# Kernel optimization log

Measured on AMD Instinct MI355X. Metric: run time of the kernel, lower is better.

Reference implementation:

```python
import jax, jax.numpy as jnp
import numpy as np

B, T, C, H = 4, 2048, 1024, 16
D = C // H

def setup_inputs() -> dict:
    key = jax.random.key(0)
    ks = jax.random.split(key, 9)
    s = 0.02
    return {
        "x": jax.random.normal(ks[0], (B, T, C), dtype=jnp.float32),
        "Wq": jax.random.normal(ks[1], (C, C), dtype=jnp.float32) * s,
        "bq": jnp.zeros((C,), dtype=jnp.float32),
        "Wk": jax.random.normal(ks[2], (C, C), dtype=jnp.float32) * s,
        "bk": jnp.zeros((C,), dtype=jnp.float32),
        "Wv": jax.random.normal(ks[3], (C, C), dtype=jnp.float32) * s,
        "bv": jnp.zeros((C,), dtype=jnp.float32),
        "Wo": jax.random.normal(ks[4], (C, C), dtype=jnp.float32) * s,
        "bo": jnp.zeros((C,), dtype=jnp.float32),
    }

def reference(x, Wq, bq, Wk, bk, Wv, bv, Wo, bo):
    # torch nn.Linear: y = x @ W.T + b
    q = x @ Wq.T + bq  # (B,T,C)
    k = x @ Wk.T + bk
    v = x @ Wv.T + bv
    # (B,H,T,D)
    q = q.reshape(B, T, H, D).transpose(0, 2, 1, 3)
    k = k.reshape(B, T, H, D).transpose(0, 2, 1, 3)
    v = v.reshape(B, T, H, D).transpose(0, 2, 1, 3)
    scale = 1.0 / jnp.sqrt(jnp.asarray(D, dtype=q.dtype))
    att = jnp.einsum("bhqd,bhkd->bhqk", q, k) * scale  # (B,H,T,T)
    causal = jnp.tril(jnp.ones((T, T), dtype=bool))
    att = jnp.where(causal[None, None], att, jnp.asarray(-jnp.inf, dtype=att.dtype))
    att = jax.nn.softmax(att, axis=-1)
    y = jnp.einsum("bhqk,bhkd->bhqd", att, v)  # (B,H,T,D)
    y = y.transpose(0, 2, 1, 3).reshape(B, T, C)
    return y @ Wo.T + bo
```

## Files before the change

### kernel.cpp

```cpp
#include <hip/hip_runtime.h>
#include <hip/hip_bf16.h>
#include <stdint.h>

typedef unsigned short u16;
typedef __bf16 bf16x8 __attribute__((ext_vector_type(8)));
typedef float f32x4 __attribute__((ext_vector_type(4)));
typedef float f32x16 __attribute__((ext_vector_type(16)));

#define NB 4
#define NT 2048
#define NC 1024
#define NH 16
#define ND 64
#define NM 8192
#define KVB 64

__device__ __forceinline__ u16 f2bf(float f) {
  union { float f; uint32_t u; } v; v.f = f;
  return (u16)((v.u + 0x7FFFu + ((v.u >> 16) & 1u)) >> 16);
}

__device__ __forceinline__ uint32_t pk2(float a, float b) {
  union { __hip_bfloat162 h; uint32_t u; } c;
  c.h = __float22bfloat162_rn(float2{a, b});
  return c.u;
}

__device__ __forceinline__ float fexp2(float x) {
#if __has_builtin(__builtin_amdgcn_exp2f)
  return __builtin_amdgcn_exp2f(x);
#else
  return exp2f(x);
#endif
}

__device__ __forceinline__ void g2l16(const void* g, void* l) {
  __builtin_amdgcn_global_load_lds((__attribute__((address_space(1))) const void*)g,
                                   (__attribute__((address_space(3))) void*)l,
                                   16, 0, 0);
}

__global__ __launch_bounds__(256) void cvt4(const float* __restrict__ in,
                                            u16* __restrict__ out, int n4) {
  int i = blockIdx.x * 256 + threadIdx.x;
  if (i >= n4) return;
  float4 v = ((const float4*)in)[i];
  ushort4 o;
  o.x = f2bf(v.x); o.y = f2bf(v.y); o.z = f2bf(v.z); o.w = f2bf(v.w);
  ((ushort4*)out)[i] = o;
}

__global__ __launch_bounds__(256) void cvtW(const float* __restrict__ w0,
                                            const float* __restrict__ w1,
                                            const float* __restrict__ w2,
                                            const float* __restrict__ w3,
                                            u16* o0, u16* o1, u16* o2, u16* o3) {
  const int y = blockIdx.y;
  const float* in = (y == 0) ? w0 : (y == 1) ? w1 : (y == 2) ? w2 : w3;
  u16* out = (y == 0) ? o0 : (y == 1) ? o1 : (y == 2) ? o2 : o3;
  int i = blockIdx.x * 256 + threadIdx.x;
  float4 v = ((const float4*)in)[i];
  ushort4 o;
  o.x = f2bf(v.x); o.y = f2bf(v.y); o.z = f2bf(v.z); o.w = f2bf(v.w);
  ((ushort4*)out)[i] = o;
}

template <int EPI>
__global__ __launch_bounds__(512, 6) void gemmQ(
    const u16* __restrict__ A,
    const u16* __restrict__ W0, const u16* __restrict__ W1, const u16* __restrict__ W2,
    const float* __restrict__ b0, const float* __restrict__ b1, const float* __restrict__ b2,
    void* o0, void* o1, void* o2, int M, int N, int K) {
  const int z = blockIdx.z;
  const u16* Bw = (z == 0) ? W0 : ((z == 1) ? W1 : W2);
  const float* bias = (z == 0) ? b0 : ((z == 1) ? b1 : b2);
  void* outp = (z == 0) ? o0 : ((z == 1) ? o1 : o2);

  __shared__ __align__(16) char SB[3 * 16384];

  const int nbn = N >> 7;
  const int lb = (blockIdx.x & 7) * (gridDim.x >> 3) + (blockIdx.x >> 3);
  const int m0 = (lb / nbn) << 7;
  const int n0 = (lb % nbn) << 7;
  const int t = threadIdx.x;
  const int wid = t >> 6, lane = t & 63;
  const int wm = wid >> 2, wn = wid & 3;
  const int lo = lane & 15, hi = lane >> 4;

  const int rw = t >> 2;
  const int chs = (((t & 3) ^ (rw & 3) ^ ((rw >> 2) & 3)) << 3);
  const u16* Asrc0 = A + (size_t)(m0 + rw) * K + chs;
  const u16* Bsrc0 = Bw + (size_t)(n0 + rw) * K + chs;
  const int ldsoff = t * 16;

  f32x4 acc[4][2];
#pragma unroll
  for (int f = 0; f < 4; ++f)
#pragma unroll
    for (int g = 0; g < 2; ++g) acc[f][g] = f32x4{0.f, 0.f, 0.f, 0.f};

  const int NTILES = K >> 5;

  auto STAGE = [&](int buf, int kt) {
    g2l16(Asrc0 + kt * 32, SB + buf * 16384 + ldsoff);
    g2l16(Bsrc0 + kt * 32, SB + buf * 16384 + 8192 + ldsoff);
  };

  STAGE(0, 0);
  STAGE(1, 1);

  int cur = 0;
  for (int kt = 0; kt < NTILES; ++kt) {
    if (kt == NTILES - 1)
      asm volatile("s_waitcnt vmcnt(0)" ::: "memory");
    else
      asm volatile("s_waitcnt vmcnt(2)" ::: "memory");
    __builtin_amdgcn_sched_barrier(0);
    asm volatile("s_barrier" ::: "memory");
    __builtin_amdgcn_sched_barrier(0);

    if (kt + 2 < NTILES) {
      int nb = cur + 2;
      if (nb >= 3) nb -= 3;
      STAGE(nb, kt + 2);
    }

    const char* Ab = SB + cur * 16384;
    const char* Bb = SB + cur * 16384 + 8192;
    bf16x8 af[4], bfr[2];
#pragma unroll
    for (int f = 0; f < 4; ++f) {
      const int row = wm * 64 + f * 16 + lo;
      af[f] = *(const bf16x8*)(Ab + row * 64 + ((hi ^ (row & 3) ^ ((row >> 2) & 3)) << 4));
    }
#pragma unroll
    for (int g = 0; g < 2; ++g) {
      const int row = wn * 32 + g * 16 + lo;
      bfr[g] = *(const bf16x8*)(Bb + row * 64 + ((hi ^ (row & 3) ^ ((row >> 2) & 3)) << 4));
    }
    __builtin_amdgcn_s_setprio(1);
#pragma unroll
    for (int f = 0; f < 4; ++f)
#pragma unroll
      for (int g = 0; g < 2; ++g)
        acc[f][g] = __builtin_amdgcn_mfma_f32_16x16x32_bf16(af[f], bfr[g],
                                                            acc[f][g], 0, 0, 0);
    __builtin_amdgcn_s_setprio(0);
    cur = (cur + 1 == 3) ? 0 : cur + 1;
  }

  const float scl = (EPI == 0 && z == 0) ? 0.125f * 1.44269504089f : 1.0f;
#pragma unroll
  for (int f = 0; f < 4; ++f) {
#pragma unroll
    for (int g = 0; g < 2; ++g) {
#pragma unroll
      for (int r = 0; r < 4; ++r) {
        const int rg = m0 + wm * 64 + f * 16 + hi * 4 + r;
        const int cg = n0 + wn * 32 + g * 16 + lo;
        const float v = (acc[f][g][r] + bias[cg]) * scl;
        if (EPI == 0) {
          const int bb = rg >> 11, tt = rg & (NT - 1);
          const int hh = cg >> 6, dd = cg & (ND - 1);
          size_t idx;
          if (z == 2)
            idx = ((size_t)(bb * NH + hh) * ND + dd) * NT + tt;
          else
            idx = ((size_t)(bb * NH + hh) * NT + tt) * ND + dd;
          ((u16*)outp)[idx] = f2bf(v);
        } else {
          ((float*)outp)[(size_t)rg * N + cg] = v;
        }
      }
    }
  }
}

__global__ __launch_bounds__(512, 4) void flash5(const u16* __restrict__ Q,
                                                 const u16* __restrict__ Kg,
                                                 const u16* __restrict__ Vtg,
                                                 u16* __restrict__ Y) {
  __shared__ __align__(16) char LDS[65536];

  const int n = blockIdx.x;
  const int xcd = n & 7, slot = n >> 3;
  const int bh = (xcd << 3) | (slot >> 3);
  const int pt = slot & 7;
  const int qtB = 15 - pt;
  const int bb = bh >> 4, hh = bh & (NH - 1);
  const int tid = threadIdx.x;
  const int lane = tid & 63;
  const int grp = tid >> 8;
  const int ws4 = (tid >> 6) & 3;
  const int ql = lane & 31, h5 = lane >> 5;
  const int swz = (ql & 7) << 4;

  const u16* Qb = Q + (size_t)bh * NT * ND;
  const u16* Kb = Kg + (size_t)bh * NT * ND;
  const u16* Vb = Vtg + (size_t)bh * ND * NT;

  const int ntA = 2 * pt + 2;
  const int kvb1 = 15 - 2 * pt;
  const int q0wB = (qtB << 7) + (ws4 << 5);

  int q0w = grp ? q0wB : (pt << 7) + (ws4 << 5);
  int qg = q0w + ql;

  bf16x8 qf[4];
#pragma unroll
  for (int s = 0; s < 4; ++s)
    qf[s] = *(const bf16x8*)(Qb + (size_t)qg * ND + s * 16 + h5 * 8);

  f32x16 O0 = 0.f, O1 = 0.f;
  float lr = 0.f;

  const int tl = tid & 255;
  char* myL = LDS + (grp << 15);

  auto kvof = [&](int it) {
    return grp ? (kvb1 + it) : (it < ntA ? it : it - ntA);
  };

  auto STAGE = [&](int buf, int kv) {
#pragma unroll
    for (int p = 0; p < 2; ++p) {
      const int c = tl + (p << 8);
      const int row = c >> 3;
      const int so = ((c & 7) << 4) ^ ((row & 7) << 4);
      g2l16((const char*)(Kb + (size_t)((kv << 6) + row) * ND) + so,
            myL + (buf << 14) + c * 16);
      g2l16((const char*)(Vb + (size_t)row * NT + (kv << 6)) + so,
            myL + (buf << 14) + 8192 + c * 16);
    }
  };

  auto WRITEY = [&](const f32x16& A0, const f32x16& A1, float inv, int qgl) {
    u16* Yb = Y + ((size_t)bb * NT + qgl) * NC + hh * ND;
#pragma unroll
    for (int rq = 0; rq < 16; rq += 4) {
      const int dbase = 2 * rq + 4 * h5;
      uint2 w2;
      w2.x = pk2(A0[rq] * inv, A0[rq + 1] * inv);
      w2.y = pk2(A0[rq + 2] * inv, A0[rq + 3] * inv);
      *(uint2*)(Yb + dbase) = w2;
      w2.x = pk2(A1[rq] * inv, A1[rq + 1] * inv);
      w2.y = pk2(A1[rq + 2] * inv, A1[rq + 3] * inv);
      *(uint2*)(Yb + 32 + dbase) = w2;
    }
  };

  STAGE(0, kvof(0));
  __syncthreads();

  for (int it = 0; it < 17; ++it) {
    const int buf = it & 1;
    if (it < 16) STAGE(buf ^ 1, kvof(it + 1));

    if (!grp && it == ntA) {
      const float lt = lr + __shfl_xor(lr, 32, 64);
      WRITEY(O0, O1, 1.f / lt, qg);
      O0 = 0.f; O1 = 0.f; lr = 0.f;
      q0w = q0wB; qg = q0w + ql;
#pragma unroll
      for (int s = 0; s < 4; ++s)
        qf[s] = *(const bf16x8*)(Qb + (size_t)qg * ND + s * 16 + h5 * 8);
    }

    const int kv0 = kvof(it) << 6;
    const char* Kc = myL + (buf << 14);
    const char* Vc = Kc + 8192;

    f32x16 Sa0 = 0.f, Sa1 = 0.f;
    __builtin_amdgcn_s_setprio(1);
#pragma unroll
    for (int s = 0; s < 4; ++s) {
      bf16x8 kf0 = *(const bf16x8*)(Kc + ql * 128 + ((s * 32 + h5 * 16) ^ swz));
      bf16x8 kf1 = *(const bf16x8*)(Kc + (32 + ql) * 128 + ((s * 32 + h5 * 16) ^ swz));
      Sa0 = __builtin_amdgcn_mfma_f32_32x32x16_bf16(kf0, qf[s], Sa0, 0, 0, 0);
      Sa1 = __builtin_amdgcn_mfma_f32_32x32x16_bf16(kf1, qf[s], Sa1, 0, 0, 0);
    }
    __builtin_amdgcn_s_setprio(0);

    if (kv0 + 63 > q0w) {
#pragma unroll
      for (int r = 0; r < 16; ++r) {
        const int kvb = kv0 + (r & 3) + 8 * (r >> 2) + 4 * h5;
        if (kvb > qg) Sa0[r] = -3e38f;
        if (kvb + 32 > qg) Sa1[r] = -3e38f;
      }
    }

    float t0 = 0.f, t1 = 0.f, t2 = 0.f, t3 = 0.f;
#pragma unroll
    for (int r = 0; r < 16; r += 4) {
      const float a0 = fexp2(Sa0[r]),     a1 = fexp2(Sa0[r + 1]);
      const float a2 = fexp2(Sa0[r + 2]), a3 = fexp2(Sa0[r + 3]);
      const float b0 = fexp2(Sa1[r]),     b1 = fexp2(Sa1[r + 1]);
      const float b2 = fexp2(Sa1[r + 2]), b3 = fexp2(Sa1[r + 3]);
      Sa0[r] = a0; Sa0[r + 1] = a1; Sa0[r + 2] = a2; Sa0[r + 3] = a3;
      Sa1[r] = b0; Sa1[r + 1] = b1; Sa1[r + 2] = b2; Sa1[r + 3] = b3;
      t0 += a0 + b0; t1 += a1 + b1; t2 += a2 + b2; t3 += a3 + b3;
    }
    lr += (t0 + t1) + (t2 + t3);

    __builtin_amdgcn_s_setprio(1);
#pragma unroll
    for (int ks = 0; ks < 4; ++ks) {
      const int k0 = ks & 1;
      const f32x16& Sk = (ks < 2) ? Sa0 : Sa1;
      const uint32_t a0 = pk2(Sk[8 * k0],     Sk[8 * k0 + 1]);
      const uint32_t a1 = pk2(Sk[8 * k0 + 2], Sk[8 * k0 + 3]);
      const uint32_t b0 = pk2(Sk[8 * k0 + 4], Sk[8 * k0 + 5]);
      const uint32_t b1 = pk2(Sk[8 * k0 + 6], Sk[8 * k0 + 7]);
      const uint32_t c0 = h5 ? b0 : a0, c1 = h5 ? b1 : a1;
      const uint32_t d0 = h5 ? a0 : b0, d1 = h5 ? a1 : b1;
      const uint32_t x0 = __shfl_xor(d0, 32, 64);
      const uint32_t x1 = __shfl_xor(d1, 32, 64);
      union { uint32_t u[4]; bf16x8 v; } pf;
      pf.u[0] = h5 ? x0 : c0;
      pf.u[1] = h5 ? x1 : c1;
      pf.u[2] = h5 ? c0 : x0;
      pf.u[3] = h5 ? c1 : x1;
      bf16x8 vf0 = *(const bf16x8*)(Vc + ql * 128 + ((ks * 32 + h5 * 16) ^ swz));
      bf16x8 vf1 = *(const bf16x8*)(Vc + (32 + ql) * 128 + ((ks * 32 + h5 * 16) ^ swz));
      O0 = __builtin_amdgcn_mfma_f32_32x32x16_bf16(vf0, pf.v, O0, 0, 0, 0);
      O1 = __builtin_amdgcn_mfma_f32_32x32x16_bf16(vf1, pf.v, O1, 0, 0, 0);
    }
    __builtin_amdgcn_s_setprio(0);

    __syncthreads();
  }

  const int cslot = (ws4 << 6) + lane;
  char* cb = LDS + cslot * 136;
  if (!grp) {
#pragma unroll
    for (int j = 0; j < 8; ++j) {
      *(float2*)(cb + j * 8)      = float2{O0[2 * j], O0[2 * j + 1]};
      *(float2*)(cb + 64 + j * 8) = float2{O1[2 * j], O1[2 * j + 1]};
    }
    *(float*)(cb + 128) = lr;
  }
  __syncthreads();
  if (grp) {
#pragma unroll
    for (int j = 0; j < 8; ++j) {
      const float2 u = *(const float2*)(cb + j * 8);
      const float2 v = *(const float2*)(cb + 64 + j * 8);
      O0[2 * j] += u.x; O0[2 * j + 1] += u.y;
      O1[2 * j] += v.x; O1[2 * j + 1] += v.y;
    }
    lr += *(const float*)(cb + 128);
    const float lt = lr + __shfl_xor(lr, 32, 64);
    WRITEY(O0, O1, 1.f / lt, qg);
  }
}

extern "C" void kernel_launch(void* const* d_in, const int* in_sizes, int n_in,
                              void* d_out, int out_size, void* d_ws, size_t ws_size,
                              hipStream_t stream) {
  const float* x  = (const float*)d_in[0];
  const float* Wq = (const float*)d_in[1];
  const float* bq = (const float*)d_in[2];
  const float* Wk = (const float*)d_in[3];
  const float* bk = (const float*)d_in[4];
  const float* Wv = (const float*)d_in[5];
  const float* bv = (const float*)d_in[6];
  const float* Wo = (const float*)d_in[7];
  const float* bo = (const float*)d_in[8];

  const size_t SZ_X = (size_t)NM * NC * 2;
  const size_t SZ_W = (size_t)NC * NC * 2;
  char* ws = (char*)d_ws;
  u16* xb  = (u16*)ws;
  u16* wqb = (u16*)(ws + SZ_X);
  u16* wkb = (u16*)(ws + SZ_X + 1 * SZ_W);
  u16* wvb = (u16*)(ws + SZ_X + 2 * SZ_W);
  u16* wob = (u16*)(ws + SZ_X + 3 * SZ_W);
  u16* vb  = (u16*)(ws + SZ_X + 4 * SZ_W);
  u16* yb  = (u16*)(ws + 2 * SZ_X + 4 * SZ_W);
  u16* qb = (u16*)d_out;
  u16* kb = (u16*)((char*)d_out + SZ_X);

  if (ws_size < 3 * SZ_X + 4 * SZ_W) return;

  cvt4<<<dim3(NM * NC / 4 / 256), 256, 0, stream>>>(x, xb, NM * NC / 4);
  cvtW<<<dim3(NC * NC / 4 / 256, 4), 256, 0, stream>>>(Wq, Wk, Wv, Wo,
                                                       wqb, wkb, wvb, wob);

  gemmQ<0><<<dim3(512, 1, 3), 512, 0, stream>>>(
      xb, wqb, wkb, wvb, bq, bk, bv, qb, kb, vb, NM, NC, NC);

  flash5<<<dim3(512), 512, 0, stream>>>(qb, kb, vb, yb);

  gemmQ<1><<<dim3(512, 1, 1), 512, 0, stream>>>(
      yb, wob, wob, wob, bo, bo, bo, d_out, d_out, d_out, NM, NC, NC);
}
```

Before: 171.3 us.

## Replace GEMM with larger-tile double-buffered kernel using 64-wide K steps

Swaps the 128x128-tile, triple-buffered, K=32 GEMM for a new kernel with 256-row tiles (256 or 128 columns) and 64-wide K steps in double-buffered LDS. Global-to-LDS loads for the next tile are interleaved between MFMA phases with finer-grained waitcnt and barrier points. The goal is higher arithmetic intensity per LDS load and fewer barriers per FLOP for the QKV and output projections. In exchange there are fewer blocks, higher register and LDS use (launch bounds lowered to 2 blocks), and more complex hand-scheduled synchronization.

```diff
diff --git a/kernel.cpp b/kernel.cpp
--- a/kernel.cpp
+++ b/kernel.cpp
@@ -65,99 +65,178 @@
   ((ushort4*)out)[i] = o;
 }
 
-template <int EPI>
-__global__ __launch_bounds__(512, 6) void gemmQ(
+template <int BN, int EPI>
+__global__ __launch_bounds__(512, 2) void gemm8(
     const u16* __restrict__ A,
     const u16* __restrict__ W0, const u16* __restrict__ W1, const u16* __restrict__ W2,
     const float* __restrict__ b0, const float* __restrict__ b1, const float* __restrict__ b2,
-    void* o0, void* o1, void* o2, int M, int N, int K) {
+    void* o0, void* o1, void* o2, int K) {
   const int z = blockIdx.z;
   const u16* Bw = (z == 0) ? W0 : ((z == 1) ? W1 : W2);
   const float* bias = (z == 0) ? b0 : ((z == 1) ? b1 : b2);
   void* outp = (z == 0) ? o0 : ((z == 1) ? o1 : o2);
 
-  __shared__ __align__(16) char SB[3 * 16384];
-
-  const int nbn = N >> 7;
+  constexpr int BUFSZ = 32768 + BN * 128;
+  constexpr int GF = BN / 64;
+  __shared__ __align__(16) char SB[2 * BUFSZ];
+
+  const int nbn = 1024 / BN;
   const int lb = (blockIdx.x & 7) * (gridDim.x >> 3) + (blockIdx.x >> 3);
-  const int m0 = (lb / nbn) << 7;
-  const int n0 = (lb % nbn) << 7;
+  const int m0 = (lb / nbn) << 8;
+  const int n0 = (lb % nbn) * BN;
   const int t = threadIdx.x;
   const int wid = t >> 6, lane = t & 63;
   const int wm = wid >> 2, wn = wid & 3;
   const int lo = lane & 15, hi = lane >> 4;
 
-  const int rw = t >> 2;
-  const int chs = (((t & 3) ^ (rw & 3) ^ ((rw >> 2) & 3)) << 3);
-  const u16* Asrc0 = A + (size_t)(m0 + rw) * K + chs;
-  const u16* Bsrc0 = Bw + (size_t)(n0 + rw) * K + chs;
-  const int ldsoff = t * 16;
-
-  f32x4 acc[4][2];
-#pragma unroll
-  for (int f = 0; f < 4; ++f)
-#pragma unroll
-    for (int g = 0; g < 2; ++g) acc[f][g] = f32x4{0.f, 0.f, 0.f, 0.f};
-
-  const int NTILES = K >> 5;
-
-  auto STAGE = [&](int buf, int kt) {
-    g2l16(Asrc0 + kt * 32, SB + buf * 16384 + ldsoff);
-    g2l16(Bsrc0 + kt * 32, SB + buf * 16384 + 8192 + ldsoff);
+  const int rr = t >> 3;
+  const int sc = ((t & 7) ^ (rr & 7)) << 3;
+  const u16* Asrc = A + (size_t)(m0 + rr) * K + sc;
+  const u16* Bsrc = Bw + (size_t)(n0 + rr) * K + sc;
+
+  f32x4 acc[8][GF] = {};
+
+  auto STA = [&](int buf, int kt, int u) {
+    g2l16(Asrc + (size_t)(u * 64) * K + kt * 64, SB + buf * BUFSZ + u * 8192 + t * 16);
   };
-
-  STAGE(0, 0);
-  STAGE(1, 1);
-
-  int cur = 0;
+  auto STB = [&](int buf, int kt, int u) {
+    g2l16(Bsrc + (size_t)(u * 64) * K + kt * 64,
+          SB + buf * BUFSZ + 32768 + u * 8192 + t * 16);
+  };
+
+  if (BN == 256) {
+    STA(0, 0, 0); STA(0, 0, 2); STB(0, 0, 0); STB(0, 0, 1);
+    STB(0, 0, 2); STB(0, 0, 3); STA(0, 0, 1); STA(0, 0, 3);
+  } else {
+    STA(0, 0, 0); STA(0, 0, 2); STB(0, 0, 0); STB(0, 0, 1);
+    STA(0, 0, 1); STA(0, 0, 3);
+  }
+
+  const int slotk[2] = {(hi ^ (lo & 7)) << 4, ((4 | hi) ^ (lo & 7)) << 4};
+  const int NTILES = K >> 6;
+
+  bf16x8 af[4][2], bfv[GF][2];
+
   for (int kt = 0; kt < NTILES; ++kt) {
-    if (kt == NTILES - 1)
-      asm volatile("s_waitcnt vmcnt(0)" ::: "memory");
-    else
-      asm volatile("s_waitcnt vmcnt(2)" ::: "memory");
+    const int cur = kt & 1, nxt = cur ^ 1;
+    const bool st = (kt + 1 < NTILES);
+    const char* Ab = SB + cur * BUFSZ;
+    const char* Bb = Ab + 32768;
+
+    asm volatile("s_waitcnt vmcnt(2)" ::: "memory");
     __builtin_amdgcn_sched_barrier(0);
     asm volatile("s_barrier" ::: "memory");
     __builtin_amdgcn_sched_barrier(0);
-
-    if (kt + 2 < NTILES) {
-      int nb = cur + 2;
-      if (nb >= 3) nb -= 3;
-      STAGE(nb, kt + 2);
-    }
-
-    const char* Ab = SB + cur * 16384;
-    const char* Bb = SB + cur * 16384 + 8192;
-    bf16x8 af[4], bfr[2];
-#pragma unroll
-    for (int f = 0; f < 4; ++f) {
-      const int row = wm * 64 + f * 16 + lo;
-      af[f] = *(const bf16x8*)(Ab + row * 64 + ((hi ^ (row & 3) ^ ((row >> 2) & 3)) << 4));
-    }
-#pragma unroll
-    for (int g = 0; g < 2; ++g) {
-      const int row = wn * 32 + g * 16 + lo;
-      bfr[g] = *(const bf16x8*)(Bb + row * 64 + ((hi ^ (row & 3) ^ ((row >> 2) & 3)) << 4));
+#pragma unroll
+    for (int f = 0; f < 4; ++f)
+#pragma unroll
+      for (int kh = 0; kh < 2; ++kh)
+        af[f][kh] = *(const bf16x8*)(Ab + (wm * 128 + f * 16 + lo) * 128 + slotk[kh]);
+#pragma unroll
+    for (int g = 0; g < 2; ++g)
+#pragma unroll
+      for (int kh = 0; kh < 2; ++kh)
+        bfv[g][kh] = *(const bf16x8*)(Bb + (wn * (BN / 4) + g * 16 + lo) * 128 + slotk[kh]);
+    if (st) {
+      STA(nxt, kt + 1, 0); STA(nxt, kt + 1, 2);
+      if (BN == 128) STB(nxt, kt + 1, 0);
     }
     __builtin_amdgcn_s_setprio(1);
 #pragma unroll
-    for (int f = 0; f < 4; ++f)
-#pragma unroll
-      for (int g = 0; g < 2; ++g)
-        acc[f][g] = __builtin_amdgcn_mfma_f32_16x16x32_bf16(af[f], bfr[g],
-                                                            acc[f][g], 0, 0, 0);
+    for (int kh = 0; kh < 2; ++kh)
+#pragma unroll
+      for (int f = 0; f < 4; ++f)
+#pragma unroll
+        for (int g = 0; g < 2; ++g)
+          acc[f][g] = __builtin_amdgcn_mfma_f32_16x16x32_bf16(af[f][kh], bfv[g][kh],
+                                                              acc[f][g], 0, 0, 0);
     __builtin_amdgcn_s_setprio(0);
-    cur = (cur + 1 == 3) ? 0 : cur + 1;
+
+    if (BN == 256) {
+#pragma unroll
+      for (int g = 2; g < 4; ++g)
+#pragma unroll
+        for (int kh = 0; kh < 2; ++kh)
+          bfv[g][kh] = *(const bf16x8*)(Bb + (wn * 64 + g * 16 + lo) * 128 + slotk[kh]);
+      if (st) { STB(nxt, kt + 1, 0); STB(nxt, kt + 1, 1); }
+      __builtin_amdgcn_s_setprio(1);
+#pragma unroll
+      for (int kh = 0; kh < 2; ++kh)
+#pragma unroll
+        for (int f = 0; f < 4; ++f)
+#pragma unroll
+          for (int g = 2; g < 4; ++g)
+            acc[f][g] = __builtin_amdgcn_mfma_f32_16x16x32_bf16(af[f][kh], bfv[g][kh],
+                                                                acc[f][g], 0, 0, 0);
+      __builtin_amdgcn_s_setprio(0);
+
+      if (st) asm volatile("s_waitcnt vmcnt(4)" ::: "memory");
+      else    asm volatile("s_waitcnt vmcnt(0)" ::: "memory");
+      __builtin_amdgcn_sched_barrier(0);
+      asm volatile("s_barrier" ::: "memory");
+      __builtin_amdgcn_sched_barrier(0);
+#pragma unroll
+      for (int f = 0; f < 4; ++f)
+#pragma unroll
+        for (int kh = 0; kh < 2; ++kh)
+          af[f][kh] = *(const bf16x8*)(Ab + (wm * 128 + (4 + f) * 16 + lo) * 128 + slotk[kh]);
+      if (st) { STB(nxt, kt + 1, 2); STB(nxt, kt + 1, 3); }
+      __builtin_amdgcn_s_setprio(1);
+#pragma unroll
+      for (int kh = 0; kh < 2; ++kh)
+#pragma unroll
+        for (int f = 0; f < 4; ++f)
+#pragma unroll
+          for (int g = 2; g < 4; ++g)
+            acc[4 + f][g] = __builtin_amdgcn_mfma_f32_16x16x32_bf16(af[f][kh], bfv[g][kh],
+                                                                    acc[4 + f][g], 0, 0, 0);
+      __builtin_amdgcn_s_setprio(0);
+
+      if (st) { STA(nxt, kt + 1, 1); STA(nxt, kt + 1, 3); }
+      __builtin_amdgcn_s_setprio(1);
+#pragma unroll
+      for (int kh = 0; kh < 2; ++kh)
+#pragma unroll
+        for (int f = 0; f < 4; ++f)
+#pragma unroll
+          for (int g = 0; g < 2; ++g)
+            acc[4 + f][g] = __builtin_amdgcn_mfma_f32_16x16x32_bf16(af[f][kh], bfv[g][kh],
+                                                                    acc[4 + f][g], 0, 0, 0);
+      __builtin_amdgcn_s_setprio(0);
+    } else {
+      if (st) asm volatile("s_waitcnt vmcnt(3)" ::: "memory");
+      else    asm volatile("s_waitcnt vmcnt(0)" ::: "memory");
+      __builtin_amdgcn_sched_barrier(0);
+      asm volatile("s_barrier" ::: "memory");
+      __builtin_amdgcn_sched_barrier(0);
+#pragma unroll
+      for (int f = 0; f < 4; ++f)
+#pragma unroll
+        for (int kh = 0; kh < 2; ++kh)
+          af[f][kh] = *(const bf16x8*)(Ab + (wm * 128 + (4 + f) * 16 + lo) * 128 + slotk[kh]);
+      if (st) { STB(nxt, kt + 1, 1); STA(nxt, kt + 1, 1); STA(nxt, kt + 1, 3); }
+      __builtin_amdgcn_s_setprio(1);
+#pragma unroll
+      for (int kh = 0; kh < 2; ++kh)
+#pragma unroll
+        for (int f = 0; f < 4; ++f)
+#pragma unroll
+          for (int g = 0; g < 2; ++g)
+            acc[4 + f][g] = __builtin_amdgcn_mfma_f32_16x16x32_bf16(af[f][kh], bfv[g][kh],
+                                                                    acc[4 + f][g], 0, 0, 0);
+      __builtin_amdgcn_s_setprio(0);
+    }
   }
 
   const float scl = (EPI == 0 && z == 0) ? 0.125f * 1.44269504089f : 1.0f;
 #pragma unroll
-  for (int f = 0; f < 4; ++f) {
-#pragma unroll
-    for (int g = 0; g < 2; ++g) {
+  for (int f = 0; f < 8; ++f) {
+#pragma unroll
+    for (int g = 0; g < GF; ++g) {
 #pragma unroll
       for (int r = 0; r < 4; ++r) {
-        const int rg = m0 + wm * 64 + f * 16 + hi * 4 + r;
-        const int cg = n0 + wn * 32 + g * 16 + lo;
+        const int rg = m0 + wm * 128 + f * 16 + hi * 4 + r;
+        const int cg = n0 + wn * (BN / 4) + g * 16 + lo;
         const float v = (acc[f][g][r] + bias[cg]) * scl;
         if (EPI == 0) {
           const int bb = rg >> 11, tt = rg & (NT - 1);
@@ -169,7 +248,7 @@
             idx = ((size_t)(bb * NH + hh) * NT + tt) * ND + dd;
           ((u16*)outp)[idx] = f2bf(v);
         } else {
-          ((float*)outp)[(size_t)rg * N + cg] = v;
+          ((float*)outp)[(size_t)rg * NC + cg] = v;
         }
       }
     }
@@ -388,11 +467,11 @@
   cvtW<<<dim3(NC * NC / 4 / 256, 4), 256, 0, stream>>>(Wq, Wk, Wv, Wo,
                                                        wqb, wkb, wvb, wob);
 
-  gemmQ<0><<<dim3(512, 1, 3), 512, 0, stream>>>(
-      xb, wqb, wkb, wvb, bq, bk, bv, qb, kb, vb, NM, NC, NC);
+  gemm8<256, 0><<<dim3(128, 1, 3), 512, 0, stream>>>(
+      xb, wqb, wkb, wvb, bq, bk, bv, qb, kb, vb, NC);
 
   flash5<<<dim3(512), 512, 0, stream>>>(qb, kb, vb, yb);
 
-  gemmQ<1><<<dim3(512, 1, 1), 512, 0, stream>>>(
-      yb, wob, wob, wob, bo, bo, bo, d_out, d_out, d_out, NM, NC, NC);
-}
+  gemm8<128, 1><<<dim3(256, 1, 1), 512, 0, stream>>>(
+      yb, wob, wob, wob, bo, bo, bo, d_out, d_out, d_out, NC);
+}
```

After: 178.6 us. +4.2%, slower.

## Replace LDS-staged GEMM with direct global-load 256x128 tile GEMM

Applied to the files above, without the earlier changes.

Rewrites the projection GEMM so each wave loads its MFMA operands straight from global memory into registers, with no LDS staging, triple buffering or barriers. The block tile grows to 256x128 and each wave now computes a 64x64 tile, which halves the grid size, and launch bounds drop to 2 blocks per CU. This removes LDS traffic and barrier synchronisation but gives up the shared reuse of operands across waves. It therefore relies on L1/L2 caches to absorb the redundant global loads, and the larger accumulator tile raises register pressure.

```diff
diff --git a/kernel.cpp b/kernel.cpp
--- a/kernel.cpp
+++ b/kernel.cpp
@@ -66,98 +66,70 @@
 }
 
 template <int EPI>
-__global__ __launch_bounds__(512, 6) void gemmQ(
+__global__ __launch_bounds__(512, 2) void gemmN(
     const u16* __restrict__ A,
     const u16* __restrict__ W0, const u16* __restrict__ W1, const u16* __restrict__ W2,
     const float* __restrict__ b0, const float* __restrict__ b1, const float* __restrict__ b2,
-    void* o0, void* o1, void* o2, int M, int N, int K) {
+    void* o0, void* o1, void* o2, int K) {
   const int z = blockIdx.z;
   const u16* Bw = (z == 0) ? W0 : ((z == 1) ? W1 : W2);
   const float* bias = (z == 0) ? b0 : ((z == 1) ? b1 : b2);
   void* outp = (z == 0) ? o0 : ((z == 1) ? o1 : o2);
 
-  __shared__ __align__(16) char SB[3 * 16384];
-
-  const int nbn = N >> 7;
+  const int nbn = 8;
   const int lb = (blockIdx.x & 7) * (gridDim.x >> 3) + (blockIdx.x >> 3);
-  const int m0 = (lb / nbn) << 7;
+  const int m0 = (lb / nbn) << 8;
   const int n0 = (lb % nbn) << 7;
   const int t = threadIdx.x;
   const int wid = t >> 6, lane = t & 63;
-  const int wm = wid >> 2, wn = wid & 3;
+  const int wm = wid >> 1, wn = wid & 1;
   const int lo = lane & 15, hi = lane >> 4;
 
-  const int rw = t >> 2;
-  const int chs = (((t & 3) ^ (rw & 3) ^ ((rw >> 2) & 3)) << 3);
-  const u16* Asrc0 = A + (size_t)(m0 + rw) * K + chs;
-  const u16* Bsrc0 = Bw + (size_t)(n0 + rw) * K + chs;
-  const int ldsoff = t * 16;
-
-  f32x4 acc[4][2];
+  const u16* Ap[4];
+  const u16* Bp[4];
 #pragma unroll
   for (int f = 0; f < 4; ++f)
-#pragma unroll
-    for (int g = 0; g < 2; ++g) acc[f][g] = f32x4{0.f, 0.f, 0.f, 0.f};
-
-  const int NTILES = K >> 5;
-
-  auto STAGE = [&](int buf, int kt) {
-    g2l16(Asrc0 + kt * 32, SB + buf * 16384 + ldsoff);
-    g2l16(Bsrc0 + kt * 32, SB + buf * 16384 + 8192 + ldsoff);
-  };
-
-  STAGE(0, 0);
-  STAGE(1, 1);
-
-  int cur = 0;
-  for (int kt = 0; kt < NTILES; ++kt) {
-    if (kt == NTILES - 1)
-      asm volatile("s_waitcnt vmcnt(0)" ::: "memory");
-    else
-      asm volatile("s_waitcnt vmcnt(2)" ::: "memory");
-    __builtin_amdgcn_sched_barrier(0);
-    asm volatile("s_barrier" ::: "memory");
-    __builtin_amdgcn_sched_barrier(0);
-
-    if (kt + 2 < NTILES) {
-      int nb = cur + 2;
-      if (nb >= 3) nb -= 3;
-      STAGE(nb, kt + 2);
-    }
-
-    const char* Ab = SB + cur * 16384;
-    const char* Bb = SB + cur * 16384 + 8192;
-    bf16x8 af[4], bfr[2];
+    Ap[f] = A + (size_t)(m0 + wm * 64 + f * 16 + lo) * K + hi * 8;
+#pragma unroll
+  for (int g = 0; g < 4; ++g)
+    Bp[g] = Bw + (size_t)(n0 + wn * 64 + g * 16 + lo) * K + hi * 8;
+
+  f32x4 acc[4][4] = {};
+
+#pragma unroll 4
+  for (int kt = 0; kt < 16; ++kt) {
+    bf16x8 af[4][2], bfv[4][2];
 #pragma unroll
     for (int f = 0; f < 4; ++f) {
-      const int row = wm * 64 + f * 16 + lo;
-      af[f] = *(const bf16x8*)(Ab + row * 64 + ((hi ^ (row & 3) ^ ((row >> 2) & 3)) << 4));
-    }
-#pragma unroll
-    for (int g = 0; g < 2; ++g) {
-      const int row = wn * 32 + g * 16 + lo;
-      bfr[g] = *(const bf16x8*)(Bb + row * 64 + ((hi ^ (row & 3) ^ ((row >> 2) & 3)) << 4));
+      af[f][0] = *(const bf16x8*)(Ap[f] + kt * 64);
+      af[f][1] = *(const bf16x8*)(Ap[f] + kt * 64 + 32);
+    }
+#pragma unroll
+    for (int g = 0; g < 4; ++g) {
+      bfv[g][0] = *(const bf16x8*)(Bp[g] + kt * 64);
+      bfv[g][1] = *(const bf16x8*)(Bp[g] + kt * 64 + 32);
     }
     __builtin_amdgcn_s_setprio(1);
 #pragma unroll
-    for (int f = 0; f < 4; ++f)
-#pragma unroll
-      for (int g = 0; g < 2; ++g)
-        acc[f][g] = __builtin_amdgcn_mfma_f32_16x16x32_bf16(af[f], bfr[g],
-                                                            acc[f][g], 0, 0, 0);
+    for (int kh = 0; kh < 2; ++kh)
+#pragma unroll
+      for (int f = 0; f < 4; ++f)
+#pragma unroll
+        for (int g = 0; g < 4; ++g)
+          acc[f][g] = __builtin_amdgcn_mfma_f32_16x16x32_bf16(af[f][kh], bfv[g][kh],
+                                                              acc[f][g], 0, 0, 0);
     __builtin_amdgcn_s_setprio(0);
-    cur = (cur + 1 == 3) ? 0 : cur + 1;
   }
 
   const float scl = (EPI == 0 && z == 0) ? 0.125f * 1.44269504089f : 1.0f;
 #pragma unroll
   for (int f = 0; f < 4; ++f) {
 #pragma unroll
-    for (int g = 0; g < 2; ++g) {
+    for (int g = 0; g < 4; ++g) {
 #pragma unroll
       for (int r = 0; r < 4; ++r) {
         const int rg = m0 + wm * 64 + f * 16 + hi * 4 + r;
-        const int cg = n0 + wn * 32 + g * 16 + lo;
+        const int cg = n0 + wn * 64 + g * 16 + lo;
         const float v = (acc[f][g][r] + bias[cg]) * scl;
         if (EPI == 0) {
           const int bb = rg >> 11, tt = rg & (NT - 1);
@@ -169,7 +141,7 @@
             idx = ((size_t)(bb * NH + hh) * NT + tt) * ND + dd;
           ((u16*)outp)[idx] = f2bf(v);
         } else {
-          ((float*)outp)[(size_t)rg * N + cg] = v;
+          ((float*)outp)[(size_t)rg * NC + cg] = v;
         }
       }
     }
@@ -388,11 +360,11 @@
   cvtW<<<dim3(NC * NC / 4 / 256, 4), 256, 0, stream>>>(Wq, Wk, Wv, Wo,
                                                        wqb, wkb, wvb, wob);
 
-  gemmQ<0><<<dim3(512, 1, 3), 512, 0, stream>>>(
-      xb, wqb, wkb, wvb, bq, bk, bv, qb, kb, vb, NM, NC, NC);
+  gemmN<0><<<dim3(256, 1, 3), 512, 0, stream>>>(
+      xb, wqb, wkb, wvb, bq, bk, bv, qb, kb, vb, NC);
 
   flash5<<<dim3(512), 512, 0, stream>>>(qb, kb, vb, yb);
 
-  gemmQ<1><<<dim3(512, 1, 1), 512, 0, stream>>>(
-      yb, wob, wob, wob, bo, bo, bo, d_out, d_out, d_out, NM, NC, NC);
-}
+  gemmN<1><<<dim3(256, 1, 1), 512, 0, stream>>>(
+      yb, wob, wob, wob, bo, bo, bo, d_out, d_out, d_out, NC);
+}
```

Result: slower. 317.7 us (+85.4%).
